# Kernel optimization log

Hardware: AMD Instinct MI355X
Metric: run time of the kernel (lower is better)

The kernel has to match this reference:

```python
import jax, jax.numpy as jnp
import numpy as np

G_ZERO_INIT = 32.0  # g initialized to log2(g0^2 - g0)


def setup_inputs() -> dict:
    key = jax.random.key(0)
    k1, k2, k3 = jax.random.split(key, 3)
    B, L, D = 64, 16384, 64
    query = jax.random.normal(k1, (B, 1, D), dtype=jnp.float32)
    keys = jax.random.normal(k2, (B, L, D), dtype=jnp.float32)
    values = jax.random.normal(k3, (B, L, 1), dtype=jnp.float32)
    g = jnp.asarray(np.log2(G_ZERO_INIT**2 - G_ZERO_INIT), dtype=jnp.float32)
    return {"query": query, "keys": keys, "values": values, "g": g, "k": 256}


def reference(query, keys, values, g, k):
    # cosine similarity between query (B,1,D) and keys (B,L,D) -> (B,L)
    qn = query / jnp.linalg.norm(query, axis=-1, keepdims=True)
    kn = keys / jnp.linalg.norm(keys, axis=-1, keepdims=True)
    similarity = jnp.einsum("bqd,bld->bl", qn, kn) * g  # (B, L)
    # top-k select + batched gather of values
    top_sim, idx = jax.lax.top_k(similarity, k)          # (B, k) each
    values_sel = jnp.take_along_axis(values, idx[:, :, None], axis=1)  # (B, k, 1)
    weights = jax.nn.softmax(top_sim, axis=-1)           # (B, k)
    return values_sel, weights
```

## Files before the change

kernel.cpp:

```cpp
#include <hip/hip_runtime.h>
#include <math.h>

#define BATCH 64
#define LSEQ  16384
#define DIM   64
#define KSEL  256
#define KPAD  384
#define NCAND 512


__device__ __forceinline__ void reduce_hist(unsigned (*histR)[256],
                                            unsigned* hist, int t)
{
    if (t < 256) {
        unsigned h = 0;
        #pragma unroll
        for (int r = 0; r < 8; ++r) h += histR[r][t];
        hist[t] = h;
    }
    __syncthreads();
}

__device__ __forceinline__ void suffix_scan_256(const unsigned* hist,
                                                unsigned* scan,
                                                unsigned* wbase, int t)
{
    const int lane = t & 63, w4 = t >> 6;
    unsigned v = (t < 256) ? hist[t] : 0u;
    #pragma unroll
    for (int off = 1; off < 64; off <<= 1) {
        unsigned u2 = __shfl_down(v, off);
        if (lane + off < 64) v += u2;
    }
    if (t < 256 && lane == 0) wbase[w4] = v;
    __syncthreads();
    if (t < 256) {
        for (int w = w4 + 1; w < 4; ++w) v += wbase[w];
        scan[t] = v;
    }
    __syncthreads();
}

__global__ __launch_bounds__(1024) void fused_topk_kernel(
    const float* __restrict__ q,
    const float* __restrict__ keys,
    const float* __restrict__ values,
    const float* __restrict__ gp,
    float* __restrict__ out)
{
    const int b = blockIdx.x;
    const int t = threadIdx.x;

    __shared__ unsigned   skey[LSEQ];
    __shared__ unsigned   histR[8][256];
    __shared__ unsigned   hist[256];
    __shared__ unsigned   scan[256];
    __shared__ unsigned   wbase[4];
    __shared__ unsigned   cidx[NCAND];
    __shared__ ulonglong2 cand[NCAND];
    __shared__ double     wsum[4];
    __shared__ unsigned   sh_hi8, sh_k, sh_t16, ccount;

    ((unsigned*)histR)[t]        = 0u;
    ((unsigned*)histR)[t + 1024] = 0u;
    if (t == 0) { ccount = 0u; sh_hi8 = 0u; sh_k = KPAD; sh_t16 = 0u; }
    __syncthreads();

    const int lane4 = t & 3;
    const int rbase = t >> 2;
    const float4* k4 = reinterpret_cast<const float4*>(keys)
                     + (size_t)b * LSEQ * (DIM / 4);
    const float4* q4 = reinterpret_cast<const float4*>(q) + b * (DIM / 4);

    float4 qa = q4[lane4 * 4 + 0];
    float4 qb = q4[lane4 * 4 + 1];
    float4 qc = q4[lane4 * 4 + 2];
    float4 qd = q4[lane4 * 4 + 3];
    const int rep = (t >> 2) & 7;

    #pragma unroll 2
    for (int it = 0; it < 64; ++it) {
        const int row = it * 256 + rbase;
        const float4* kp = k4 + row * 16 + lane4 * 4;
        float4 ka = kp[0], kb = kp[1], kc = kp[2], kd = kp[3];

        float dot = qa.x*ka.x + qa.y*ka.y + qa.z*ka.z + qa.w*ka.w
                  + qb.x*kb.x + qb.y*kb.y + qb.z*kb.z + qb.w*kb.w
                  + qc.x*kc.x + qc.y*kc.y + qc.z*kc.z + qc.w*kc.w
                  + qd.x*kd.x + qd.y*kd.y + qd.z*kd.z + qd.w*kd.w;
        float kss = ka.x*ka.x + ka.y*ka.y + ka.z*ka.z + ka.w*ka.w
                  + kb.x*kb.x + kb.y*kb.y + kb.z*kb.z + kb.w*kb.w
                  + kc.x*kc.x + kc.y*kc.y + kc.z*kc.z + kc.w*kc.w
                  + kd.x*kd.x + kd.y*kd.y + kd.z*kd.z + kd.w*kd.w;
        dot += __shfl_xor(dot, 1); dot += __shfl_xor(dot, 2);
        kss += __shfl_xor(kss, 1); kss += __shfl_xor(kss, 2);

        if (lane4 == 0) {
            float s = dot * fabsf(dot) / kss;
            unsigned u = __float_as_uint(s);
            unsigned key = (u >> 31) ? ~u : (u | 0x80000000u);
            skey[row] = key;
            atomicAdd(&histR[rep][key >> 24], 1u);
        }
    }
    __syncthreads();

    reduce_hist(histR, hist, t);
    suffix_scan_256(hist, scan, wbase, t);
    if (t < 256 && scan[t] >= KPAD && (t == 255 || scan[t + 1] < KPAD)) {
        sh_hi8 = (unsigned)t;
        sh_k   = KPAD - ((t == 255) ? 0u : scan[t + 1]);
    }
    __syncthreads();

    ((unsigned*)histR)[t]        = 0u;
    ((unsigned*)histR)[t + 1024] = 0u;
    __syncthreads();
    const unsigned hi8  = sh_hi8;
    const unsigned kcur = sh_k;
    #pragma unroll
    for (int it = 0; it < 16; ++it) {
        unsigned key = skey[it * 1024 + t];
        if ((key >> 24) == hi8)
            atomicAdd(&histR[t & 7][(key >> 16) & 255u], 1u);
    }
    __syncthreads();
    reduce_hist(histR, hist, t);
    suffix_scan_256(hist, scan, wbase, t);
    if (t < 256 && scan[t] >= kcur && (t == 255 || scan[t + 1] < kcur))
        sh_t16 = (hi8 << 8) | (unsigned)t;
    __syncthreads();
    const unsigned T16 = sh_t16;

    #pragma unroll
    for (int it = 0; it < 16; ++it) {
        const int l = it * 1024 + t;
        unsigned key = skey[l];
        if ((key >> 16) >= T16) {
            unsigned pos = atomicAdd(&ccount, 1u);
            if (pos < NCAND) cidx[pos] = (unsigned)l;
        }
    }
    __syncthreads();
    const unsigned total = (ccount < (unsigned)NCAND) ? ccount : (unsigned)NCAND;

    const int j = t & 15;
    const float4 qv = q4[j];
    const double qx = qv.x, qy = qv.y, qz = qv.z, qw = qv.w;
    double qss = qx*qx + qy*qy + qz*qz + qw*qw;
    #pragma unroll
    for (int m = 1; m < 16; m <<= 1) qss += __shfl_xor(qss, m);
    const double scale = (double)gp[0] / sqrt(qss);

    const int cslot = t >> 4;
    for (int sweep = 0; sweep < NCAND / 64; ++sweep) {
        const int cc = sweep * 64 + cslot;
        if (cc < (int)total) {
            const int row = (int)cidx[cc];
            float4 kv = k4[row * 16 + j];
            const double kx = kv.x, ky = kv.y, kz = kv.z, kw = kv.w;
            double dot = qx*kx + qy*ky + qz*kz + qw*kw;
            double kss = kx*kx + ky*ky + kz*kz + kw*kw;
            #pragma unroll
            for (int m = 1; m < 16; m <<= 1) {
                dot += __shfl_xor(dot, m);
                kss += __shfl_xor(kss, m);
            }
            if (j == 0) {
                double sim = scale * dot / sqrt(kss);
                unsigned long long u =
                    (unsigned long long)__double_as_longlong(sim);
                unsigned long long k64 =
                    (u >> 63) ? ~u : (u | 0x8000000000000000ull);
                cand[cc] = make_ulonglong2(
                    k64, (unsigned long long)(0xFFFFFFFFu - (unsigned)row));
            }
        } else if (j == 0) {
            cand[cc] = make_ulonglong2(0ull, 0ull);
        }
    }
    __syncthreads();

    for (int size = 2; size <= NCAND; size <<= 1) {
        for (int stride = size >> 1; stride > 0; stride >>= 1) {
            __syncthreads();
            if (t < 256) {
                int i  = ((t & ~(stride - 1)) << 1) | (t & (stride - 1));
                int jj = i + stride;
                bool up = ((i & size) == 0);
                ulonglong2 a = cand[i], c = cand[jj];
                bool agt = (a.x > c.x) || (a.x == c.x && a.y > c.y);
                if (agt == up) { cand[i] = c; cand[jj] = a; }
            }
        }
    }
    __syncthreads();

    double e = 0.0;
    unsigned idx = 0u;
    if (t < 256) {
        ulonglong2 v = cand[511 - t];
        idx = 0xFFFFFFFFu - (unsigned)v.y;
        unsigned long long ub = (v.x & 0x8000000000000000ull)
                              ? (v.x ^ 0x8000000000000000ull) : ~v.x;
        double sv = __longlong_as_double((long long)ub);

        ulonglong2 vm = cand[511];
        unsigned long long um = (vm.x & 0x8000000000000000ull)
                              ? (vm.x ^ 0x8000000000000000ull) : ~vm.x;
        double fm = __longlong_as_double((long long)um);

        e = exp(sv - fm);
        double esum = e;
        #pragma unroll
        for (int m = 1; m < 64; m <<= 1) esum += __shfl_xor(esum, m);
        if ((t & 63) == 0) wsum[t >> 6] = esum;
    }
    __syncthreads();
    if (t < 256) {
        const double tot = wsum[0] + wsum[1] + wsum[2] + wsum[3];
        out[b * KSEL + t]                = values[(size_t)b * LSEQ + idx];
        out[BATCH * KSEL + b * KSEL + t] = (float)(e / tot);
    }
}

extern "C" void kernel_launch(void* const* d_in, const int* in_sizes, int n_in,
                              void* d_out, int out_size, void* d_ws, size_t ws_size,
                              hipStream_t stream)
{
    (void)d_ws; (void)ws_size;
    const float* q      = (const float*)d_in[0];
    const float* keys   = (const float*)d_in[1];
    const float* values = (const float*)d_in[2];
    const float* g      = (const float*)d_in[3];
    float* out = (float*)d_out;

    fused_topk_kernel<<<dim3(BATCH), dim3(1024), 0, stream>>>(q, keys, values, g, out);
}
```

Before: 450.5 us.

## Split similarity pass into a separate wide-grid kernel feeding top-k kernel

The fp32 similarity scoring of all keys moves out of the 64-block fused kernel into its own kernel launched with 4096 blocks of 256 threads. Scores are written as sortable keys to workspace, and the top-k kernel reloads them with vector loads to build the histogram. The point is to spread the 256 MB key read across every CU instead of only 64 blocks. The cost is an extra launch and a round trip of the 4 MB score array through global memory, and the code assumes the workspace is large enough.

```diff
diff --git a/kernel.cpp b/kernel.cpp
--- a/kernel.cpp
+++ b/kernel.cpp
@@ -9,6 +9,43 @@
 #define NCAND 512
 
 
+__global__ __launch_bounds__(256) void sim32_kernel(
+    const float* __restrict__ q,
+    const float* __restrict__ keys,
+    unsigned* __restrict__ skeys)
+{
+    const int b     = blockIdx.x >> 6;
+    const int chunk = blockIdx.x & 63;
+    const int t  = threadIdx.x;
+    const int j  = t & 15;
+    const int rl = t >> 4;
+
+    const float4* q4 = reinterpret_cast<const float4*>(q) + b * 16;
+    float4 qv = q4[j];
+    const float qx = qv.x, qy = qv.y, qz = qv.z, qw = qv.w;
+
+    const float4* k4 = reinterpret_cast<const float4*>(keys) + (size_t)b * LSEQ * 16;
+    const int row_base = chunk * 256;
+    unsigned* sk = skeys + (size_t)b * LSEQ;
+
+    for (int it = 0; it < 16; ++it) {
+        const int row = row_base + it * 16 + rl;
+        float4 kv = k4[row * 16 + j];
+        float dot = qx*kv.x + qy*kv.y + qz*kv.z + qw*kv.w;
+        float kss = kv.x*kv.x + kv.y*kv.y + kv.z*kv.z + kv.w*kv.w;
+        #pragma unroll
+        for (int m = 1; m < 16; m <<= 1) {
+            dot += __shfl_xor(dot, m);
+            kss += __shfl_xor(kss, m);
+        }
+        if (j == 0) {
+            float s = dot * fabsf(dot) / kss;
+            unsigned u = __float_as_uint(s);
+            sk[row] = (u >> 31) ? ~u : (u | 0x80000000u);
+        }
+    }
+}
+
 __device__ __forceinline__ void reduce_hist(unsigned (*histR)[256],
                                             unsigned* hist, int t)
 {
@@ -41,11 +78,12 @@
     __syncthreads();
 }
 
-__global__ __launch_bounds__(1024) void fused_topk_kernel(
+__global__ __launch_bounds__(1024) void topk_kernel(
     const float* __restrict__ q,
     const float* __restrict__ keys,
     const float* __restrict__ values,
     const float* __restrict__ gp,
+    const unsigned* __restrict__ skeys,
     float* __restrict__ out)
 {
     const int b = blockIdx.x;
@@ -66,42 +104,16 @@
     if (t == 0) { ccount = 0u; sh_hi8 = 0u; sh_k = KPAD; sh_t16 = 0u; }
     __syncthreads();
 
-    const int lane4 = t & 3;
-    const int rbase = t >> 2;
-    const float4* k4 = reinterpret_cast<const float4*>(keys)
-                     + (size_t)b * LSEQ * (DIM / 4);
-    const float4* q4 = reinterpret_cast<const float4*>(q) + b * (DIM / 4);
-
-    float4 qa = q4[lane4 * 4 + 0];
-    float4 qb = q4[lane4 * 4 + 1];
-    float4 qc = q4[lane4 * 4 + 2];
-    float4 qd = q4[lane4 * 4 + 3];
-    const int rep = (t >> 2) & 7;
-
-    #pragma unroll 2
-    for (int it = 0; it < 64; ++it) {
-        const int row = it * 256 + rbase;
-        const float4* kp = k4 + row * 16 + lane4 * 4;
-        float4 ka = kp[0], kb = kp[1], kc = kp[2], kd = kp[3];
-
-        float dot = qa.x*ka.x + qa.y*ka.y + qa.z*ka.z + qa.w*ka.w
-                  + qb.x*kb.x + qb.y*kb.y + qb.z*kb.z + qb.w*kb.w
-                  + qc.x*kc.x + qc.y*kc.y + qc.z*kc.z + qc.w*kc.w
-                  + qd.x*kd.x + qd.y*kd.y + qd.z*kd.z + qd.w*kd.w;
-        float kss = ka.x*ka.x + ka.y*ka.y + ka.z*ka.z + ka.w*ka.w
-                  + kb.x*kb.x + kb.y*kb.y + kb.z*kb.z + kb.w*kb.w
-                  + kc.x*kc.x + kc.y*kc.y + kc.z*kc.z + kc.w*kc.w
-                  + kd.x*kd.x + kd.y*kd.y + kd.z*kd.z + kd.w*kd.w;
-        dot += __shfl_xor(dot, 1); dot += __shfl_xor(dot, 2);
-        kss += __shfl_xor(kss, 1); kss += __shfl_xor(kss, 2);
-
-        if (lane4 == 0) {
-            float s = dot * fabsf(dot) / kss;
-            unsigned u = __float_as_uint(s);
-            unsigned key = (u >> 31) ? ~u : (u | 0x80000000u);
-            skey[row] = key;
-            atomicAdd(&histR[rep][key >> 24], 1u);
-        }
+    const uint4* wk4 = reinterpret_cast<const uint4*>(skeys + (size_t)b * LSEQ);
+    #pragma unroll
+    for (int it = 0; it < 4; ++it) {
+        const int i = it * 1024 + t;
+        uint4 v = wk4[i];
+        reinterpret_cast<uint4*>(skey)[i] = v;
+        atomicAdd(&histR[t & 7][v.x >> 24], 1u);
+        atomicAdd(&histR[t & 7][v.y >> 24], 1u);
+        atomicAdd(&histR[t & 7][v.z >> 24], 1u);
+        atomicAdd(&histR[t & 7][v.w >> 24], 1u);
     }
     __syncthreads();
 
@@ -144,6 +156,9 @@
     __syncthreads();
     const unsigned total = (ccount < (unsigned)NCAND) ? ccount : (unsigned)NCAND;
 
+    const float4* q4 = reinterpret_cast<const float4*>(q) + b * (DIM / 4);
+    const float4* k4 = reinterpret_cast<const float4*>(keys)
+                     + (size_t)b * LSEQ * (DIM / 4);
     const int j = t & 15;
     const float4 qv = q4[j];
     const double qx = qv.x, qy = qv.y, qz = qv.z, qw = qv.w;
@@ -228,12 +243,13 @@
                               void* d_out, int out_size, void* d_ws, size_t ws_size,
                               hipStream_t stream)
 {
-    (void)d_ws; (void)ws_size;
     const float* q      = (const float*)d_in[0];
     const float* keys   = (const float*)d_in[1];
     const float* values = (const float*)d_in[2];
     const float* g      = (const float*)d_in[3];
-    float* out = (float*)d_out;
-
-    fused_topk_kernel<<<dim3(BATCH), dim3(1024), 0, stream>>>(q, keys, values, g, out);
-}
+    float* out  = (float*)d_out;
+    unsigned* skeys = (unsigned*)d_ws;
+
+    sim32_kernel<<<dim3(BATCH * (LSEQ / 256)), dim3(256), 0, stream>>>(q, keys, skeys);
+    topk_kernel<<<dim3(BATCH), dim3(1024), 0, stream>>>(q, keys, values, g, skeys, out);
+}
```

After: 392.2 us. -12.9%, faster.
